# Optimization experiments

Measured on AMD Instinct MI355X. Metric: run time of the kernel, lower is better.

Reference implementation:

```python
import jax, jax.numpy as jnp
import numpy as np

NUM_LAYER = 5
EMB = 300
BN_EPS = 1e-5
NUM_BOND_TYPE = 6
NUM_BOND_DIR = 3
SELF_LOOP_TYPE = 4  # pretrain-gnns self-loop edge attr = [4, 0]


def setup_inputs() -> dict:
    key = jax.random.key(0)
    ks = jax.random.split(key, 12)
    N, E, D = 100000, 250000, EMB
    x = jax.random.normal(ks[0], (N, D), dtype=jnp.float32)
    edge_index = jax.random.randint(ks[1], (2, E), 0, N, dtype=jnp.int64)
    edge_attr = jax.random.randint(ks[2], (E, 2), 0, 3, dtype=jnp.int64)
    L = NUM_LAYER
    W1 = jax.random.normal(ks[3], (L, D, 2 * D), dtype=jnp.float32) * 0.05
    b1 = jnp.zeros((L, 2 * D), dtype=jnp.float32)
    W2 = jax.random.normal(ks[4], (L, 2 * D, D), dtype=jnp.float32) * 0.05
    b2 = jnp.zeros((L, D), dtype=jnp.float32)
    E1 = jax.random.normal(ks[5], (L, NUM_BOND_TYPE, D), dtype=jnp.float32) * 0.05
    E2 = jax.random.normal(ks[6], (L, NUM_BOND_DIR, D), dtype=jnp.float32) * 0.05
    gamma = jnp.ones((L, D), dtype=jnp.float32)
    beta = jnp.zeros((L, D), dtype=jnp.float32)
    return {"x": x, "edge_index": edge_index, "edge_attr": edge_attr,
            "W1": W1, "b1": b1, "W2": W2, "b2": b2,
            "E1": E1, "E2": E2, "gamma": gamma, "beta": beta}


def reference(x, edge_index, edge_attr, W1, b1, W2, b2, E1, E2, gamma, beta):
    N = x.shape[0]
    src, dst = edge_index[0], edge_index[1]
    bt, bd = edge_attr[:, 0], edge_attr[:, 1]
    h = x
    for l in range(NUM_LAYER):
        # GINEConv: message = x_j + edge_embedding, aggr='add', with self loops
        edge_emb = E1[l][bt] + E2[l][bd]                 # [E, D]
        self_emb = E1[l][SELF_LOOP_TYPE] + E2[l][0]      # [D]
        msg = h[src] + edge_emb                          # [E, D] gather
        agg = jax.ops.segment_sum(msg, dst, num_segments=N) + h + self_emb
        # update MLP: Linear(D,2D) -> ReLU -> Linear(2D,D)
        m = jax.nn.relu(agg @ W1[l] + b1[l]) @ W2[l] + b2[l]
        # BatchNorm1d in training mode (batch stats over nodes, biased var)
        mu = m.mean(axis=0)
        var = m.var(axis=0)
        m = (m - mu) * jax.lax.rsqrt(var + BN_EPS) * gamma[l] + beta[l]
        if l < NUM_LAYER - 1:  # ReLU on all but last layer; dropout ratio 0 -> no-op
            m = jax.nn.relu(m)
        h = m
    return h  # JK == 'last'
```

## Files before the change

### kernel.cpp

```cpp
#include <hip/hip_runtime.h>
#include <hip/hip_bf16.h>

#define NN 100000
#define NE 250000
#define DD 300
#define DDB 304
#define NL 5
#define MPAD 100096
#define KA1 320
#define N1 608
#define N1T 640
#define K2 608
#define N2T 384
#define NBLK 391
#define NCMB 19

typedef __attribute__((ext_vector_type(8))) short short8;
typedef __attribute__((ext_vector_type(4))) float f32x4;

#define GLBP(x) ((const __attribute__((address_space(1))) unsigned int*)(x))
#define LDSP(x) ((__attribute__((address_space(3))) unsigned int*)(x))
#define WAITV(N) asm volatile("s_waitcnt vmcnt(" #N ")" ::: "memory")

__device__ __forceinline__ ushort f2bf(float f){
  unsigned u = __float_as_uint(f);
  u += 0x7FFFu + ((u >> 16) & 1u);
  return (ushort)(u >> 16);
}
__device__ __forceinline__ float bf2f(ushort h){
  return __uint_as_float((unsigned)h << 16);
}
__device__ __forceinline__ unsigned pk2(float a, float b){
  return (unsigned)f2bf(a) | ((unsigned)f2bf(b) << 16);
}

__global__ void prep_weights(const float* __restrict__ W1, const float* __restrict__ W2,
                             ushort* __restrict__ W1T, ushort* __restrict__ W2T){
  int idx = blockIdx.x * 256 + threadIdx.x;
  const int total1 = NL * N1T * KA1;
  const int total2 = NL * N2T * K2;
  if (idx < total1){
    int l = idx / (N1T * KA1);
    int rem = idx % (N1T * KA1);
    int n = rem / KA1, k = rem % KA1;
    float v = (n < 2*DD && k < DD) ? W1[(size_t)l*DD*2*DD + (size_t)k*2*DD + n] : 0.0f;
    W1T[idx] = f2bf(v);
  } else {
    int idx2 = idx - total1;
    if (idx2 < total2){
      int l = idx2 / (N2T * K2);
      int rem = idx2 % (N2T * K2);
      int n = rem / K2, k = rem % K2;
      float v = (n < DD && k < 2*DD) ? W2[(size_t)l*2*DD*DD + (size_t)k*DD + n] : 0.0f;
      W2T[idx2] = f2bf(v);
    }
  }
}

__global__ void prep_ctab(const float* __restrict__ E1, const float* __restrict__ E2,
                          float* __restrict__ ctab){
  int idx = blockIdx.x * 256 + threadIdx.x;
  if (idx >= NL * NCMB * DDB) return;
  int l = idx / (NCMB * DDB);
  int rem = idx % (NCMB * DDB);
  int c = rem / DDB, d = rem % DDB;
  float v = 0.0f;
  if (d < DD){
    int bt = (c < 18) ? (c / 3) : 4;
    int bd = (c < 18) ? (c % 3) : 0;
    v = E1[(size_t)l*6*DD + bt*DD + d] + E2[(size_t)l*3*DD + bd*DD + d];
  }
  ctab[idx] = v;
}

__global__ void csr_count(const int* __restrict__ ei, int* __restrict__ deg){
  int e = blockIdx.x * 256 + threadIdx.x;
  if (e < NE) atomicAdd(&deg[ei[NE + e]], 1);
}

__global__ void scan_blk(const int* __restrict__ deg, int* __restrict__ rs, int* __restrict__ bsum){
  __shared__ int tmp[256];
  int i = blockIdx.x * 256 + threadIdx.x;
  int v = (i < NN) ? deg[i] : 0;
  tmp[threadIdx.x] = v;
  __syncthreads();
  #pragma unroll
  for (int off = 1; off < 256; off <<= 1){
    int t = (threadIdx.x >= off) ? tmp[threadIdx.x - off] : 0;
    __syncthreads();
    tmp[threadIdx.x] += t;
    __syncthreads();
  }
  if (i < NN) rs[i] = tmp[threadIdx.x] - v;
  if (threadIdx.x == 255) bsum[blockIdx.x] = tmp[255];
}

__global__ void scan_top(int* __restrict__ bsum){
  __shared__ int tmp[512];
  int v = (threadIdx.x < NBLK) ? bsum[threadIdx.x] : 0;
  tmp[threadIdx.x] = v;
  __syncthreads();
  #pragma unroll
  for (int off = 1; off < 512; off <<= 1){
    int t = (threadIdx.x >= off) ? tmp[threadIdx.x - off] : 0;
    __syncthreads();
    tmp[threadIdx.x] += t;
    __syncthreads();
  }
  if (threadIdx.x < NBLK) bsum[threadIdx.x] = tmp[threadIdx.x] - v;
}

__global__ void scan_add(int* __restrict__ rs, const int* __restrict__ bsum){
  int i = blockIdx.x * 256 + threadIdx.x;
  if (i < NN) rs[i] += bsum[blockIdx.x];
  if (i == 0) rs[NN] = NE;
}

__global__ void csr_fill(const int* __restrict__ ei, const int* __restrict__ ea,
                         const int* __restrict__ rs, int* __restrict__ cursor,
                         int* __restrict__ edges){
  int e = blockIdx.x * 256 + threadIdx.x;
  if (e < NE){
    int dst = ei[NE + e];
    int src = ei[e];
    int c = ea[2*e] * 3 + ea[2*e + 1];
    int p = rs[dst] + atomicAdd(&cursor[dst], 1);
    edges[p] = src | (c << 20);
  }
}

template<int HBF>
__global__ __launch_bounds__(256) void gather_agg(
    const void* __restrict__ hp, const float2* __restrict__ ss,
    const float* __restrict__ ctab_l,
    const int* __restrict__ rs, const int* __restrict__ edges,
    ushort* __restrict__ agg)
{
  int lane = threadIdx.x & 63;
  int wq = __builtin_amdgcn_readfirstlane(threadIdx.x >> 6);
  int wid = blockIdx.x * 4 + wq;
  int nw = gridDim.x * 4;
  int dA = lane * 4;
  int dB = 256 + lane * 4;
  bool laneB  = (lane < 16);
  bool validB = (dB < DD);

  float scA[4], shA[4], scB[4], shB[4];
  if (HBF){
    #pragma unroll
    for (int j = 0; j < 4; ++j){
      float2 s = ss[dA + j]; scA[j] = s.x; shA[j] = s.y;
    }
    if (validB){
      #pragma unroll
      for (int j = 0; j < 4; ++j){
        float2 s = ss[dB + j]; scB[j] = s.x; shB[j] = s.y;
      }
    }
  }

  const float*  hf = (const float*)hp;
  const ushort* hb = (const ushort*)hp;
  const float* ctS = ctab_l + 18*DDB;

  for (int row = wid; row < MPAD; row += nw){
    float a0=0,a1=0,a2=0,a3=0, b0=0,b1=0,b2=0,b3=0;
    if (row < NN){
      if (HBF){
        uint2 hw = *(const uint2*)(hb + (size_t)row*DDB + dA);
        a0 = fmaxf(bf2f((ushort)hw.x)*scA[0]+shA[0],0.f)      + ctS[dA+0];
        a1 = fmaxf(bf2f((ushort)(hw.x>>16))*scA[1]+shA[1],0.f)+ ctS[dA+1];
        a2 = fmaxf(bf2f((ushort)hw.y)*scA[2]+shA[2],0.f)      + ctS[dA+2];
        a3 = fmaxf(bf2f((ushort)(hw.y>>16))*scA[3]+shA[3],0.f)+ ctS[dA+3];
        if (validB){
          uint2 hv = *(const uint2*)(hb + (size_t)row*DDB + dB);
          b0 = fmaxf(bf2f((ushort)hv.x)*scB[0]+shB[0],0.f)      + ctS[dB+0];
          b1 = fmaxf(bf2f((ushort)(hv.x>>16))*scB[1]+shB[1],0.f)+ ctS[dB+1];
          b2 = fmaxf(bf2f((ushort)hv.y)*scB[2]+shB[2],0.f)      + ctS[dB+2];
          b3 = fmaxf(bf2f((ushort)(hv.y>>16))*scB[3]+shB[3],0.f)+ ctS[dB+3];
        }
      } else {
        float4 hv = *(const float4*)(hf + (size_t)row*DD + dA);
        a0 = hv.x + ctS[dA+0]; a1 = hv.y + ctS[dA+1];
        a2 = hv.z + ctS[dA+2]; a3 = hv.w + ctS[dA+3];
        if (validB){
          float4 hv2 = *(const float4*)(hf + (size_t)row*DD + dB);
          b0 = hv2.x + ctS[dB+0]; b1 = hv2.y + ctS[dB+1];
          b2 = hv2.z + ctS[dB+2]; b3 = hv2.w + ctS[dB+3];
        }
      }
      int p = rs[row], pe = rs[row + 1];
      for (; p < pe; ++p){
        int ew = edges[p];
        int src = ew & 0xFFFFF;
        const float* ct = ctab_l + (ew >> 20)*DDB;
        if (HBF){
          uint2 hw = *(const uint2*)(hb + (size_t)src*DDB + dA);
          a0 += fmaxf(bf2f((ushort)hw.x)*scA[0]+shA[0],0.f)      + ct[dA+0];
          a1 += fmaxf(bf2f((ushort)(hw.x>>16))*scA[1]+shA[1],0.f)+ ct[dA+1];
          a2 += fmaxf(bf2f((ushort)hw.y)*scA[2]+shA[2],0.f)      + ct[dA+2];
          a3 += fmaxf(bf2f((ushort)(hw.y>>16))*scA[3]+shA[3],0.f)+ ct[dA+3];
          if (validB){
            uint2 hv = *(const uint2*)(hb + (size_t)src*DDB + dB);
            b0 += fmaxf(bf2f((ushort)hv.x)*scB[0]+shB[0],0.f)      + ct[dB+0];
            b1 += fmaxf(bf2f((ushort)(hv.x>>16))*scB[1]+shB[1],0.f)+ ct[dB+1];
            b2 += fmaxf(bf2f((ushort)hv.y)*scB[2]+shB[2],0.f)      + ct[dB+2];
            b3 += fmaxf(bf2f((ushort)(hv.y>>16))*scB[3]+shB[3],0.f)+ ct[dB+3];
          }
        } else {
          float4 hv = *(const float4*)(hf + (size_t)src*DD + dA);
          a0 += hv.x + ct[dA+0]; a1 += hv.y + ct[dA+1];
          a2 += hv.z + ct[dA+2]; a3 += hv.w + ct[dA+3];
          if (validB){
            float4 hv2 = *(const float4*)(hf + (size_t)src*DD + dB);
            b0 += hv2.x + ct[dB+0]; b1 += hv2.y + ct[dB+1];
            b2 += hv2.z + ct[dB+2]; b3 += hv2.w + ct[dB+3];
          }
        }
      }
    }
    ushort* ag = agg + (size_t)row*KA1;
    uint2 oA; oA.x = pk2(a0, a1); oA.y = pk2(a2, a3);
    *(uint2*)(ag + dA) = oA;
    if (laneB){
      uint2 oB;
      if (validB){ oB.x = pk2(b0, b1); oB.y = pk2(b2, b3); }
      else       { oB.x = 0; oB.y = 0; }
      *(uint2*)(ag + dB) = oB;
    }
  }
}

template<int OUT_BF16, int RELU, int STATS>
__global__ __launch_bounds__(256) void gemm_lds(
    const ushort* __restrict__ A, int lda,
    const ushort* __restrict__ B, int ldb,
    void* __restrict__ Cp, int ldc,
    int kTiles, const float* __restrict__ bias, int biasN,
    int Mvalid, int Nvalid, int nColTiles, float* __restrict__ statf)
{
  __shared__ ushort As[5][4096];
  __shared__ ushort Bs[5][4096];
  int tid = threadIdx.x;
  int lane = tid & 63, w = tid >> 6;
  int wm = (w >> 1) * 64, wn = (w & 1) * 64;

  int nwg = gridDim.x;
  int q = nwg >> 3, r = nwg & 7;
  int xcd = blockIdx.x & 7, idx = blockIdx.x >> 3;
  int bid = (xcd < r ? xcd * (q + 1) : r * (q + 1) + (xcd - r) * q) + idx;
  int m0 = (bid / nColTiles) * 128;
  int n0 = (bid % nColTiles) * 128;

  int r0 = tid >> 2;
  int kc = ((tid & 3) ^ ((tid >> 3) & 3)) * 8;
  const ushort* Ap = A + (size_t)(m0 + r0)*lda + kc;
  const ushort* Bp = B + (size_t)(n0 + r0)*ldb + kc;

  f32x4 acc[4][4] = {};

#define STAGE(buf, kt) do { \
    int _ko = (kt) * 32; \
    __builtin_amdgcn_global_load_lds(GLBP(Ap + _ko),                  LDSP(&As[buf][w*512]),        16, 0, 0); \
    __builtin_amdgcn_global_load_lds(GLBP(Ap + _ko + (size_t)64*lda), LDSP(&As[buf][w*512 + 2048]), 16, 0, 0); \
    __builtin_amdgcn_global_load_lds(GLBP(Bp + _ko),                  LDSP(&Bs[buf][w*512]),        16, 0, 0); \
    __builtin_amdgcn_global_load_lds(GLBP(Bp + _ko + (size_t)64*ldb), LDSP(&Bs[buf][w*512 + 2048]), 16, 0, 0); \
  } while (0)

  STAGE(0, 0); STAGE(1, 1); STAGE(2, 2); STAGE(3, 3);
  WAITV(12);
  __builtin_amdgcn_s_barrier();

  int fr = lane & 15;
  int ko8 = (((lane >> 4) ^ ((fr >> 1) & 3))) * 8;
  int cur = 0;
  for (int kt = 0; kt < kTiles; ++kt){
    int sb = cur + 4; if (sb >= 5) sb -= 5;
    if (kt + 4 < kTiles) STAGE(sb, kt + 4);
    short8 af[4], bfv[4];
    #pragma unroll
    for (int i = 0; i < 4; ++i)
      af[i] = *(const short8*)&As[cur][(wm + i*16 + fr)*32 + ko8];
    #pragma unroll
    for (int j = 0; j < 4; ++j)
      bfv[j] = *(const short8*)&Bs[cur][(wn + j*16 + fr)*32 + ko8];
    #pragma unroll
    for (int i = 0; i < 4; ++i)
      #pragma unroll
      for (int j = 0; j < 4; ++j)
        acc[i][j] = __builtin_amdgcn_mfma_f32_16x16x32_bf16(af[i], bfv[j], acc[i][j], 0, 0, 0);
    if (kt + 1 < kTiles){
      int rem = kTiles - kt;
      if      (rem >= 5) WAITV(12);
      else if (rem == 4) WAITV(8);
      else if (rem == 3) WAITV(4);
      else               WAITV(0);
      __builtin_amdgcn_s_barrier();
    }
    cur = cur + 1; if (cur >= 5) cur = 0;
  }
#undef STAGE

  int cc = lane & 15, cr = (lane >> 4) * 4;
  float ps[4], pq[4];
  if (STATS){
    #pragma unroll
    for (int j = 0; j < 4; ++j){ ps[j] = 0.0f; pq[j] = 0.0f; }
  }
  #pragma unroll
  for (int i = 0; i < 4; ++i){
    #pragma unroll
    for (int j = 0; j < 4; ++j){
      int col = n0 + wn + j*16 + cc;
      if (col >= Nvalid) continue;
      float bv = (col < biasN) ? bias[col] : 0.0f;
      #pragma unroll
      for (int r2 = 0; r2 < 4; ++r2){
        int row = m0 + wm + i*16 + cr + r2;
        if (row < Mvalid){
          float v = acc[i][j][r2] + bv;
          if (RELU) v = fmaxf(v, 0.0f);
          if (OUT_BF16) ((ushort*)Cp)[(size_t)row*ldc + col] = f2bf(v);
          else          ((float*) Cp)[(size_t)row*ldc + col] = v;
          if (STATS){ ps[j] += v; pq[j] += v * v; }
        }
      }
    }
  }
  if (STATS){
    #pragma unroll
    for (int j = 0; j < 4; ++j){
      float s = ps[j], qv = pq[j];
      s += __shfl_xor(s, 16); qv += __shfl_xor(qv, 16);
      s += __shfl_xor(s, 32); qv += __shfl_xor(qv, 32);
      int col = n0 + wn + j*16 + cc;
      if ((lane >> 4) == 0 && col < Nvalid){
        unsafeAtomicAdd(&statf[col], s);
        unsafeAtomicAdd(&statf[N2T + col], qv);
      }
    }
  }
}

__global__ void make_norm(const float* __restrict__ statf, const float* __restrict__ gamma,
                          const float* __restrict__ beta, float2* __restrict__ ss){
  int d = threadIdx.x;
  if (d >= DD) return;
  double mu = (double)statf[d] / (double)NN;
  double var = (double)statf[N2T + d] / (double)NN - mu * mu;
  float inv = rsqrtf((float)var + 1e-5f);
  float sc = inv * gamma[d];
  ss[d] = make_float2(sc, beta[d] - (float)mu * sc);
}

__global__ void apply_norm(const float* __restrict__ m2, const float2* __restrict__ ss,
                           float* __restrict__ out){
  int row = blockIdx.x;
  int d = threadIdx.x;
  if (d >= DD) return;
  float2 s = ss[d];
  out[(size_t)row*DD + d] = m2[(size_t)row*DD + d] * s.x + s.y;
}

extern "C" void kernel_launch(void* const* d_in, const int* in_sizes, int n_in,
                              void* d_out, int out_size, void* d_ws, size_t ws_size,
                              hipStream_t stream) {
  const float* x     = (const float*)d_in[0];
  const int*   ei    = (const int*)  d_in[1];
  const int*   ea    = (const int*)  d_in[2];
  const float* W1    = (const float*)d_in[3];
  const float* b1    = (const float*)d_in[4];
  const float* W2    = (const float*)d_in[5];
  const float* b2    = (const float*)d_in[6];
  const float* E1    = (const float*)d_in[7];
  const float* E2    = (const float*)d_in[8];
  const float* gamma = (const float*)d_in[9];
  const float* beta  = (const float*)d_in[10];

  char* p = (char*)d_ws;
  float*  m2buf = (float*) p; p += (size_t)NN * DD * 4;
  ushort* m2bf  = (ushort*)p; p += (size_t)NN * DDB * 2;
  ushort* agg   = (ushort*)p; p += (size_t)MPAD * KA1 * 2;
  ushort* m1    = (ushort*)p; p += (size_t)MPAD * N1 * 2;
  ushort* W1T   = (ushort*)p; p += (size_t)NL * N1T * KA1 * 2;
  ushort* W2T   = (ushort*)p; p += (size_t)NL * N2T * K2 * 2;
  float*  ctab  = (float*) p; p += (size_t)NL * NCMB * DDB * 4;
  int*    deg   = (int*)   p; p += (size_t)NN * 4;
  int*    rs    = (int*)   p; p += (size_t)(NN + 16) * 4;
  int*    bsum  = (int*)   p; p += (size_t)512 * 4;
  int*    cursor= (int*)   p; p += (size_t)NN * 4;
  int*    edges = (int*)   p; p += (size_t)NE * 4;
  float*  statf = (float*) p; p += (size_t)2 * N2T * 4;
  float2* ss    = (float2*)p;

  {
    int total = NL*N1T*KA1 + NL*N2T*K2;
    prep_weights<<<(total + 255)/256, 256, 0, stream>>>(W1, W2, W1T, W2T);
    int tc = NL * NCMB * DDB;
    prep_ctab<<<(tc + 255)/256, 256, 0, stream>>>(E1, E2, ctab);
  }
  hipMemsetAsync(deg, 0, (size_t)NN*4, stream);
  hipMemsetAsync(cursor, 0, (size_t)NN*4, stream);
  csr_count<<<(NE + 255)/256, 256, 0, stream>>>(ei, deg);
  scan_blk<<<NBLK, 256, 0, stream>>>(deg, rs, bsum);
  scan_top<<<1, 512, 0, stream>>>(bsum);
  scan_add<<<NBLK, 256, 0, stream>>>(rs, bsum);
  csr_fill<<<(NE + 255)/256, 256, 0, stream>>>(ei, ea, rs, cursor, edges);

  for (int l = 0; l < NL; ++l){
    const float* ctab_l = ctab + (size_t)l * NCMB * DDB;

    if (l == 0)
      gather_agg<0><<<1024, 256, 0, stream>>>(x, nullptr, ctab_l, rs, edges, agg);
    else
      gather_agg<1><<<1024, 256, 0, stream>>>(m2bf, ss, ctab_l, rs, edges, agg);

    gemm_lds<1,1,0><<<(MPAD/128) * (N1T/128), 256, 0, stream>>>(
        agg, KA1, W1T + (size_t)l*N1T*KA1, KA1, m1, N1, KA1/32,
        b1 + (size_t)l*2*DD, 2*DD, MPAD, N1, N1T/128, nullptr);

    hipMemsetAsync(statf, 0, (size_t)2*N2T*4, stream);

    if (l < NL - 1)
      gemm_lds<1,0,1><<<(MPAD/128) * (N2T/128), 256, 0, stream>>>(
          m1, N1, W2T + (size_t)l*N2T*K2, K2, m2bf, DDB, K2/32,
          b2 + (size_t)l*DD, DD, NN, DD, N2T/128, statf);
    else
      gemm_lds<0,0,1><<<(MPAD/128) * (N2T/128), 256, 0, stream>>>(
          m1, N1, W2T + (size_t)l*N2T*K2, K2, m2buf, DD, K2/32,
          b2 + (size_t)l*DD, DD, NN, DD, N2T/128, statf);

    make_norm<<<1, 320, 0, stream>>>(statf, gamma + (size_t)l*DD, beta + (size_t)l*DD, ss);
  }
  apply_norm<<<NN, 320, 0, stream>>>(m2buf, ss, (float*)d_out);
}
```

Before: 1.888 ms.

## Add 256-row GEMM tile variant for second MLP layer and double gather grid

Adds a 512-thread GEMM kernel with 256x128 output tiles and a 3-stage LDS pipeline, used for the second MLP linear layer (K=608, N=384). Each B tile is now shared by twice as many rows, and the grid has fewer workgroups. The gather/aggregate kernel launch also doubles from 1024 to 2048 blocks to expose more parallelism. The costs are a shallower pipeline (3 stages instead of 5) and more LDS per block, which may lower occupancy.

```diff
diff --git a/kernel.cpp b/kernel.cpp
--- a/kernel.cpp
+++ b/kernel.cpp
@@ -232,7 +232,7 @@
 }
 
 template<int OUT_BF16, int RELU, int STATS>
-__global__ __launch_bounds__(256) void gemm_lds(
+__global__ __launch_bounds__(256) void gemm_128(
     const ushort* __restrict__ A, int lda,
     const ushort* __restrict__ B, int ldb,
     void* __restrict__ Cp, int ldc,
@@ -298,6 +298,114 @@
       __builtin_amdgcn_s_barrier();
     }
     cur = cur + 1; if (cur >= 5) cur = 0;
+  }
+#undef STAGE
+
+  int cc = lane & 15, cr = (lane >> 4) * 4;
+  float ps[4], pq[4];
+  if (STATS){
+    #pragma unroll
+    for (int j = 0; j < 4; ++j){ ps[j] = 0.0f; pq[j] = 0.0f; }
+  }
+  #pragma unroll
+  for (int i = 0; i < 4; ++i){
+    #pragma unroll
+    for (int j = 0; j < 4; ++j){
+      int col = n0 + wn + j*16 + cc;
+      if (col >= Nvalid) continue;
+      float bv = (col < biasN) ? bias[col] : 0.0f;
+      #pragma unroll
+      for (int r2 = 0; r2 < 4; ++r2){
+        int row = m0 + wm + i*16 + cr + r2;
+        if (row < Mvalid){
+          float v = acc[i][j][r2] + bv;
+          if (RELU) v = fmaxf(v, 0.0f);
+          if (OUT_BF16) ((ushort*)Cp)[(size_t)row*ldc + col] = f2bf(v);
+          else          ((float*) Cp)[(size_t)row*ldc + col] = v;
+          if (STATS){ ps[j] += v; pq[j] += v * v; }
+        }
+      }
+    }
+  }
+  if (STATS){
+    #pragma unroll
+    for (int j = 0; j < 4; ++j){
+      float s = ps[j], qv = pq[j];
+      s += __shfl_xor(s, 16); qv += __shfl_xor(qv, 16);
+      s += __shfl_xor(s, 32); qv += __shfl_xor(qv, 32);
+      int col = n0 + wn + j*16 + cc;
+      if ((lane >> 4) == 0 && col < Nvalid){
+        unsafeAtomicAdd(&statf[col], s);
+        unsafeAtomicAdd(&statf[N2T + col], qv);
+      }
+    }
+  }
+}
+
+template<int OUT_BF16, int RELU, int STATS>
+__global__ __launch_bounds__(512) void gemm_256(
+    const ushort* __restrict__ A, int lda,
+    const ushort* __restrict__ B, int ldb,
+    void* __restrict__ Cp, int ldc,
+    int kTiles, const float* __restrict__ bias, int biasN,
+    int Mvalid, int Nvalid, int nColTiles, float* __restrict__ statf)
+{
+  __shared__ ushort As[3][8192];
+  __shared__ ushort Bs[3][4096];
+  int tid = threadIdx.x;
+  int lane = tid & 63, w = tid >> 6;
+  int wm = (w >> 1) * 64, wn = (w & 1) * 64;
+
+  int nwg = gridDim.x;
+  int q = nwg >> 3, r = nwg & 7;
+  int xcd = blockIdx.x & 7, idx = blockIdx.x >> 3;
+  int bid = (xcd < r ? xcd * (q + 1) : r * (q + 1) + (xcd - r) * q) + idx;
+  int m0 = (bid / nColTiles) * 256;
+  int n0 = (bid % nColTiles) * 128;
+
+  int r0 = tid >> 2;
+  int kc = ((tid & 3) ^ ((tid >> 3) & 3)) * 8;
+  const ushort* Ap = A + (size_t)(m0 + r0)*lda + kc;
+  const ushort* Bp = B + (size_t)(n0 + r0)*ldb + kc;
+
+  f32x4 acc[4][4] = {};
+
+#define STAGE(buf, kt) do { \
+    int _ko = (kt) * 32; \
+    __builtin_amdgcn_global_load_lds(GLBP(Ap + _ko),                   LDSP(&As[buf][w*512]),        16, 0, 0); \
+    __builtin_amdgcn_global_load_lds(GLBP(Ap + _ko + (size_t)128*lda), LDSP(&As[buf][w*512 + 4096]), 16, 0, 0); \
+    __builtin_amdgcn_global_load_lds(GLBP(Bp + _ko),                   LDSP(&Bs[buf][w*512]),        16, 0, 0); \
+  } while (0)
+
+  STAGE(0, 0);
+  STAGE(1, 1);
+  WAITV(3);
+  __builtin_amdgcn_s_barrier();
+
+  int fr = lane & 15;
+  int ko8 = (((lane >> 4) ^ ((fr >> 1) & 3))) * 8;
+  int cur = 0;
+  for (int kt = 0; kt < kTiles; ++kt){
+    int sb = cur + 2; if (sb >= 3) sb -= 3;
+    if (kt + 2 < kTiles) STAGE(sb, kt + 2);
+    short8 af[4], bfv[4];
+    #pragma unroll
+    for (int i = 0; i < 4; ++i)
+      af[i] = *(const short8*)&As[cur][(wm + i*16 + fr)*32 + ko8];
+    #pragma unroll
+    for (int j = 0; j < 4; ++j)
+      bfv[j] = *(const short8*)&Bs[cur][(wn + j*16 + fr)*32 + ko8];
+    #pragma unroll
+    for (int i = 0; i < 4; ++i)
+      #pragma unroll
+      for (int j = 0; j < 4; ++j)
+        acc[i][j] = __builtin_amdgcn_mfma_f32_16x16x32_bf16(af[i], bfv[j], acc[i][j], 0, 0, 0);
+    if (kt + 1 < kTiles){
+      if (kt + 2 < kTiles) WAITV(3);
+      else                 WAITV(0);
+      __builtin_amdgcn_s_barrier();
+    }
+    cur = cur + 1; if (cur >= 3) cur = 0;
   }
 #undef STAGE
 
@@ -411,22 +519,22 @@
     const float* ctab_l = ctab + (size_t)l * NCMB * DDB;
 
     if (l == 0)
-      gather_agg<0><<<1024, 256, 0, stream>>>(x, nullptr, ctab_l, rs, edges, agg);
+      gather_agg<0><<<2048, 256, 0, stream>>>(x, nullptr, ctab_l, rs, edges, agg);
     else
-      gather_agg<1><<<1024, 256, 0, stream>>>(m2bf, ss, ctab_l, rs, edges, agg);
-
-    gemm_lds<1,1,0><<<(MPAD/128) * (N1T/128), 256, 0, stream>>>(
+      gather_agg<1><<<2048, 256, 0, stream>>>(m2bf, ss, ctab_l, rs, edges, agg);
+
+    gemm_128<1,1,0><<<(MPAD/128) * (N1T/128), 256, 0, stream>>>(
         agg, KA1, W1T + (size_t)l*N1T*KA1, KA1, m1, N1, KA1/32,
         b1 + (size_t)l*2*DD, 2*DD, MPAD, N1, N1T/128, nullptr);
 
     hipMemsetAsync(statf, 0, (size_t)2*N2T*4, stream);
 
     if (l < NL - 1)
-      gemm_lds<1,0,1><<<(MPAD/128) * (N2T/128), 256, 0, stream>>>(
+      gemm_256<1,0,1><<<(MPAD/256) * (N2T/128), 512, 0, stream>>>(
           m1, N1, W2T + (size_t)l*N2T*K2, K2, m2bf, DDB, K2/32,
           b2 + (size_t)l*DD, DD, NN, DD, N2T/128, statf);
     else
-      gemm_lds<0,0,1><<<(MPAD/128) * (N2T/128), 256, 0, stream>>>(
+      gemm_256<0,0,1><<<(MPAD/256) * (N2T/128), 512, 0, stream>>>(
           m1, N1, W2T + (size_t)l*N2T*K2, K2, m2buf, DD, K2/32,
           b2 + (size_t)l*DD, DD, NN, DD, N2T/128, statf);
 
```

Measured after the change: 1.753 ms. 7.1% less time.

## Fuse the two MLP GEMMs into one kernel keeping the hidden tile in LDS

Applied to the files above, without the earlier changes.

Replaces the two separate GEMM launches with a single 512-thread kernel. Each block owns 128 rows, computes the 640-wide hidden layer in 128-column chunks, applies bias and ReLU into an LDS tile, and accumulates the second GEMM over all 384 output columns in registers. This removes the global round trip of the 100k x 608 bf16 intermediate and one launch per layer. In exchange it needs large LDS and register use, which lowers occupancy, and only 782 blocks are launched. The gather kernel grid is also doubled.

```diff
diff --git a/kernel.cpp b/kernel.cpp
--- a/kernel.cpp
+++ b/kernel.cpp
@@ -8,10 +8,9 @@
 #define NL 5
 #define MPAD 100096
 #define KA1 320
-#define N1 608
 #define N1T 640
-#define K2 608
 #define N2T 384
+#define K2P 640
 #define NBLK 391
 #define NCMB 19
 
@@ -38,7 +37,7 @@
                              ushort* __restrict__ W1T, ushort* __restrict__ W2T){
   int idx = blockIdx.x * 256 + threadIdx.x;
   const int total1 = NL * N1T * KA1;
-  const int total2 = NL * N2T * K2;
+  const int total2 = NL * N2T * K2P;
   if (idx < total1){
     int l = idx / (N1T * KA1);
     int rem = idx % (N1T * KA1);
@@ -48,9 +47,9 @@
   } else {
     int idx2 = idx - total1;
     if (idx2 < total2){
-      int l = idx2 / (N2T * K2);
-      int rem = idx2 % (N2T * K2);
-      int n = rem / K2, k = rem % K2;
+      int l = idx2 / (N2T * K2P);
+      int rem = idx2 % (N2T * K2P);
+      int n = rem / K2P, k = rem % K2P;
       float v = (n < DD && k < 2*DD) ? W2[(size_t)l*2*DD*DD + (size_t)k*DD + n] : 0.0f;
       W2T[idx2] = f2bf(v);
     }
@@ -164,7 +163,7 @@
   const float* ctS = ctab_l + 18*DDB;
 
   for (int row = wid; row < MPAD; row += nw){
-    float a0=0,a1=0,a2=0,a3=0, b0=0,b1=0,b2=0,b3=0;
+    float a0=0,a1=0,a2=0,a3=0, b0=0,b1v=0,b2v=0,b3=0;
     if (row < NN){
       if (HBF){
         uint2 hw = *(const uint2*)(hb + (size_t)row*DDB + dA);
@@ -174,10 +173,10 @@
         a3 = fmaxf(bf2f((ushort)(hw.y>>16))*scA[3]+shA[3],0.f)+ ctS[dA+3];
         if (validB){
           uint2 hv = *(const uint2*)(hb + (size_t)row*DDB + dB);
-          b0 = fmaxf(bf2f((ushort)hv.x)*scB[0]+shB[0],0.f)      + ctS[dB+0];
-          b1 = fmaxf(bf2f((ushort)(hv.x>>16))*scB[1]+shB[1],0.f)+ ctS[dB+1];
-          b2 = fmaxf(bf2f((ushort)hv.y)*scB[2]+shB[2],0.f)      + ctS[dB+2];
-          b3 = fmaxf(bf2f((ushort)(hv.y>>16))*scB[3]+shB[3],0.f)+ ctS[dB+3];
+          b0  = fmaxf(bf2f((ushort)hv.x)*scB[0]+shB[0],0.f)      + ctS[dB+0];
+          b1v = fmaxf(bf2f((ushort)(hv.x>>16))*scB[1]+shB[1],0.f)+ ctS[dB+1];
+          b2v = fmaxf(bf2f((ushort)hv.y)*scB[2]+shB[2],0.f)      + ctS[dB+2];
+          b3  = fmaxf(bf2f((ushort)(hv.y>>16))*scB[3]+shB[3],0.f)+ ctS[dB+3];
         }
       } else {
         float4 hv = *(const float4*)(hf + (size_t)row*DD + dA);
@@ -185,8 +184,8 @@
         a2 = hv.z + ctS[dA+2]; a3 = hv.w + ctS[dA+3];
         if (validB){
           float4 hv2 = *(const float4*)(hf + (size_t)row*DD + dB);
-          b0 = hv2.x + ctS[dB+0]; b1 = hv2.y + ctS[dB+1];
-          b2 = hv2.z + ctS[dB+2]; b3 = hv2.w + ctS[dB+3];
+          b0 = hv2.x + ctS[dB+0]; b1v = hv2.y + ctS[dB+1];
+          b2v = hv2.z + ctS[dB+2]; b3 = hv2.w + ctS[dB+3];
         }
       }
       int p = rs[row], pe = rs[row + 1];
@@ -202,10 +201,10 @@
           a3 += fmaxf(bf2f((ushort)(hw.y>>16))*scA[3]+shA[3],0.f)+ ct[dA+3];
           if (validB){
             uint2 hv = *(const uint2*)(hb + (size_t)src*DDB + dB);
-            b0 += fmaxf(bf2f((ushort)hv.x)*scB[0]+shB[0],0.f)      + ct[dB+0];
-            b1 += fmaxf(bf2f((ushort)(hv.x>>16))*scB[1]+shB[1],0.f)+ ct[dB+1];
-            b2 += fmaxf(bf2f((ushort)hv.y)*scB[2]+shB[2],0.f)      + ct[dB+2];
-            b3 += fmaxf(bf2f((ushort)(hv.y>>16))*scB[3]+shB[3],0.f)+ ct[dB+3];
+            b0  += fmaxf(bf2f((ushort)hv.x)*scB[0]+shB[0],0.f)      + ct[dB+0];
+            b1v += fmaxf(bf2f((ushort)(hv.x>>16))*scB[1]+shB[1],0.f)+ ct[dB+1];
+            b2v += fmaxf(bf2f((ushort)hv.y)*scB[2]+shB[2],0.f)      + ct[dB+2];
+            b3  += fmaxf(bf2f((ushort)(hv.y>>16))*scB[3]+shB[3],0.f)+ ct[dB+3];
           }
         } else {
           float4 hv = *(const float4*)(hf + (size_t)src*DD + dA);
@@ -213,8 +212,8 @@
           a2 += hv.z + ct[dA+2]; a3 += hv.w + ct[dA+3];
           if (validB){
             float4 hv2 = *(const float4*)(hf + (size_t)src*DD + dB);
-            b0 += hv2.x + ct[dB+0]; b1 += hv2.y + ct[dB+1];
-            b2 += hv2.z + ct[dB+2]; b3 += hv2.w + ct[dB+3];
+            b0 += hv2.x + ct[dB+0]; b1v += hv2.y + ct[dB+1];
+            b2v += hv2.z + ct[dB+2]; b3 += hv2.w + ct[dB+3];
           }
         }
       }
@@ -224,120 +223,177 @@
     *(uint2*)(ag + dA) = oA;
     if (laneB){
       uint2 oB;
-      if (validB){ oB.x = pk2(b0, b1); oB.y = pk2(b2, b3); }
+      if (validB){ oB.x = pk2(b0, b1v); oB.y = pk2(b2v, b3); }
       else       { oB.x = 0; oB.y = 0; }
       *(uint2*)(ag + dB) = oB;
     }
   }
 }
 
-template<int OUT_BF16, int RELU, int STATS>
-__global__ __launch_bounds__(256) void gemm_lds(
-    const ushort* __restrict__ A, int lda,
-    const ushort* __restrict__ B, int ldb,
+template<int OUT_BF16>
+__global__ __launch_bounds__(512) void mlp_fused(
+    const ushort* __restrict__ agg,
+    const ushort* __restrict__ W1T_l,
+    const ushort* __restrict__ W2T_l,
+    const float* __restrict__ b1_l,
+    const float* __restrict__ b2_l,
     void* __restrict__ Cp, int ldc,
-    int kTiles, const float* __restrict__ bias, int biasN,
-    int Mvalid, int Nvalid, int nColTiles, float* __restrict__ statf)
+    float* __restrict__ statf)
 {
-  __shared__ ushort As[5][4096];
-  __shared__ ushort Bs[5][4096];
+  __shared__ ushort Sa[3][4096];
+  __shared__ ushort Sb[3][4096];
+  __shared__ ushort Ws[3][12288];
+  __shared__ ushort Pt[16384];
+
   int tid = threadIdx.x;
   int lane = tid & 63, w = tid >> 6;
-  int wm = (w >> 1) * 64, wn = (w & 1) * 64;
+  int wmA = (w >> 2) * 64;
+  int wnA = (w & 3) * 32;
+  int wnB = (w & 3) * 96;
 
   int nwg = gridDim.x;
   int q = nwg >> 3, r = nwg & 7;
-  int xcd = blockIdx.x & 7, idx = blockIdx.x >> 3;
-  int bid = (xcd < r ? xcd * (q + 1) : r * (q + 1) + (xcd - r) * q) + idx;
-  int m0 = (bid / nColTiles) * 128;
-  int n0 = (bid % nColTiles) * 128;
+  int xcd = blockIdx.x & 7, bix = blockIdx.x >> 3;
+  int bid = (xcd < r ? xcd*(q+1) : r*(q+1) + (xcd-r)*q) + bix;
+  int m0 = bid * 128;
 
   int r0 = tid >> 2;
   int kc = ((tid & 3) ^ ((tid >> 3) & 3)) * 8;
-  const ushort* Ap = A + (size_t)(m0 + r0)*lda + kc;
-  const ushort* Bp = B + (size_t)(n0 + r0)*ldb + kc;
-
-  f32x4 acc[4][4] = {};
-
-#define STAGE(buf, kt) do { \
+  const ushort* Ap = agg + (size_t)(m0 + r0)*KA1 + kc;
+
+  int fr = lane & 15;
+  int kq = lane >> 4;
+  int ko8 = (kq ^ ((fr >> 1) & 3)) * 8;
+  int cc = lane & 15, cr = kq * 4;
+
+  f32x4 acc2[4][6] = {};
+
+#define STAGE_A(buf, kt) do { \
     int _ko = (kt) * 32; \
-    __builtin_amdgcn_global_load_lds(GLBP(Ap + _ko),                  LDSP(&As[buf][w*512]),        16, 0, 0); \
-    __builtin_amdgcn_global_load_lds(GLBP(Ap + _ko + (size_t)64*lda), LDSP(&As[buf][w*512 + 2048]), 16, 0, 0); \
-    __builtin_amdgcn_global_load_lds(GLBP(Bp + _ko),                  LDSP(&Bs[buf][w*512]),        16, 0, 0); \
-    __builtin_amdgcn_global_load_lds(GLBP(Bp + _ko + (size_t)64*ldb), LDSP(&Bs[buf][w*512 + 2048]), 16, 0, 0); \
+    __builtin_amdgcn_global_load_lds(GLBP(Ap + _ko),  LDSP(&Sa[buf][w*512]), 16, 0, 0); \
+    __builtin_amdgcn_global_load_lds(GLBP(W1p + _ko), LDSP(&Sb[buf][w*512]), 16, 0, 0); \
   } while (0)
-
-  STAGE(0, 0); STAGE(1, 1); STAGE(2, 2); STAGE(3, 3);
-  WAITV(12);
-  __builtin_amdgcn_s_barrier();
-
-  int fr = lane & 15;
-  int ko8 = (((lane >> 4) ^ ((fr >> 1) & 3))) * 8;
-  int cur = 0;
-  for (int kt = 0; kt < kTiles; ++kt){
-    int sb = cur + 4; if (sb >= 5) sb -= 5;
-    if (kt + 4 < kTiles) STAGE(sb, kt + 4);
-    short8 af[4], bfv[4];
+#define STAGE_W(buf, s) do { \
+    int _ko = (s) * 32; \
+    __builtin_amdgcn_global_load_lds(GLBP(W2p + _ko),                   LDSP(&Ws[buf][w*512]),        16, 0, 0); \
+    __builtin_amdgcn_global_load_lds(GLBP(W2p + _ko + (size_t)128*K2P), LDSP(&Ws[buf][w*512 + 4096]), 16, 0, 0); \
+    __builtin_amdgcn_global_load_lds(GLBP(W2p + _ko + (size_t)256*K2P), LDSP(&Ws[buf][w*512 + 8192]), 16, 0, 0); \
+  } while (0)
+
+  #pragma unroll 1
+  for (int jb = 0; jb < 5; ++jb){
+    const ushort* W1p = W1T_l + (size_t)(jb*128 + r0)*KA1 + kc;
+    const ushort* W2p = W2T_l + (size_t)r0*K2P + jb*128 + kc;
+
+    f32x4 accA[4][2] = {};
+    STAGE_A(0, 0); STAGE_A(1, 1);
+    WAITV(2);
+    __builtin_amdgcn_s_barrier();
+    int cur = 0;
+    for (int kt = 0; kt < 10; ++kt){
+      int sb = cur + 2; if (sb >= 3) sb -= 3;
+      if (kt + 2 < 10) STAGE_A(sb, kt + 2);
+      short8 af[4], bw[2];
+      #pragma unroll
+      for (int i = 0; i < 4; ++i)
+        af[i] = *(const short8*)&Sa[cur][(wmA + i*16 + fr)*32 + ko8];
+      #pragma unroll
+      for (int j2 = 0; j2 < 2; ++j2)
+        bw[j2] = *(const short8*)&Sb[cur][(wnA + j2*16 + fr)*32 + ko8];
+      #pragma unroll
+      for (int i = 0; i < 4; ++i)
+        #pragma unroll
+        for (int j2 = 0; j2 < 2; ++j2)
+          accA[i][j2] = __builtin_amdgcn_mfma_f32_16x16x32_bf16(af[i], bw[j2], accA[i][j2], 0, 0, 0);
+      if (kt + 1 < 10){
+        if (kt + 2 < 10) WAITV(2);
+        else             WAITV(0);
+        __builtin_amdgcn_s_barrier();
+      }
+      cur = cur + 1; if (cur >= 3) cur = 0;
+    }
     #pragma unroll
-    for (int i = 0; i < 4; ++i)
-      af[i] = *(const short8*)&As[cur][(wm + i*16 + fr)*32 + ko8];
+    for (int i = 0; i < 4; ++i){
+      #pragma unroll
+      for (int j2 = 0; j2 < 2; ++j2){
+        int pcol = wnA + j2*16 + cc;
+        int gcol = jb*128 + pcol;
+        float bv = (gcol < 2*DD) ? b1_l[gcol] : 0.0f;
+        #pragma unroll
+        for (int r2 = 0; r2 < 4; ++r2){
+          int prow = wmA + i*16 + cr + r2;
+          float v = fmaxf(accA[i][j2][r2] + bv, 0.0f);
+          int gp = (pcol >> 3) ^ ((prow >> 1) & 7);
+          Pt[prow*128 + gp*8 + (pcol & 7)] = f2bf(v);
+        }
+      }
+    }
+    STAGE_W(0, 0); STAGE_W(1, 1);
+    asm volatile("s_waitcnt lgkmcnt(0)" ::: "memory");
+    __builtin_amdgcn_sched_barrier(0);
+    __builtin_amdgcn_s_barrier();
+    WAITV(3);
+    __builtin_amdgcn_s_barrier();
+
     #pragma unroll
-    for (int j = 0; j < 4; ++j)
-      bfv[j] = *(const short8*)&Bs[cur][(wn + j*16 + fr)*32 + ko8];
-    #pragma unroll
-    for (int i = 0; i < 4; ++i)
-      #pragma unroll
-      for (int j = 0; j < 4; ++j)
-        acc[i][j] = __builtin_amdgcn_mfma_f32_16x16x32_bf16(af[i], bfv[j], acc[i][j], 0, 0, 0);
-    if (kt + 1 < kTiles){
-      int rem = kTiles - kt;
-      if      (rem >= 5) WAITV(12);
-      else if (rem == 4) WAITV(8);
-      else if (rem == 3) WAITV(4);
-      else               WAITV(0);
+    for (int s = 0; s < 4; ++s){
+      if (s + 2 < 4) STAGE_W((s + 2) % 3, s + 2);
+      if      (s == 1) WAITV(6);
+      else if (s == 2) WAITV(3);
+      else if (s == 3) WAITV(0);
+      if (s) __builtin_amdgcn_s_barrier();
+      short8 pf[4], wf[6];
+      #pragma unroll
+      for (int i = 0; i < 4; ++i){
+        int prow = wmA + i*16 + fr;
+        int gp = (s*4 + kq) ^ ((prow >> 1) & 7);
+        pf[i] = *(const short8*)&Pt[prow*128 + gp*8];
+      }
+      #pragma unroll
+      for (int j2 = 0; j2 < 6; ++j2)
+        wf[j2] = *(const short8*)&Ws[s % 3][(wnB + j2*16 + fr)*32 + ko8];
+      #pragma unroll
+      for (int i = 0; i < 4; ++i)
+        #pragma unroll
+        for (int j2 = 0; j2 < 6; ++j2)
+          acc2[i][j2] = __builtin_amdgcn_mfma_f32_16x16x32_bf16(pf[i], wf[j2], acc2[i][j2], 0, 0, 0);
       __builtin_amdgcn_s_barrier();
     }
-    cur = cur + 1; if (cur >= 5) cur = 0;
-  }
-#undef STAGE
-
-  int cc = lane & 15, cr = (lane >> 4) * 4;
-  float ps[4], pq[4];
-  if (STATS){
-    #pragma unroll
-    for (int j = 0; j < 4; ++j){ ps[j] = 0.0f; pq[j] = 0.0f; }
-  }
+  }
+#undef STAGE_A
+#undef STAGE_W
+
+  float ps[6], pq[6];
+  #pragma unroll
+  for (int j2 = 0; j2 < 6; ++j2){ ps[j2] = 0.0f; pq[j2] = 0.0f; }
   #pragma unroll
   for (int i = 0; i < 4; ++i){
     #pragma unroll
-    for (int j = 0; j < 4; ++j){
-      int col = n0 + wn + j*16 + cc;
-      if (col >= Nvalid) continue;
-      float bv = (col < biasN) ? bias[col] : 0.0f;
+    for (int j2 = 0; j2 < 6; ++j2){
+      int col = wnB + j2*16 + cc;
+      if (col >= DD) continue;
+      float bv = b2_l[col];
       #pragma unroll
       for (int r2 = 0; r2 < 4; ++r2){
-        int row = m0 + wm + i*16 + cr + r2;
-        if (row < Mvalid){
-          float v = acc[i][j][r2] + bv;
-          if (RELU) v = fmaxf(v, 0.0f);
+        int row = m0 + wmA + i*16 + cr + r2;
+        if (row < NN){
+          float v = acc2[i][j2][r2] + bv;
           if (OUT_BF16) ((ushort*)Cp)[(size_t)row*ldc + col] = f2bf(v);
           else          ((float*) Cp)[(size_t)row*ldc + col] = v;
-          if (STATS){ ps[j] += v; pq[j] += v * v; }
+          ps[j2] += v; pq[j2] += v * v;
         }
       }
     }
   }
-  if (STATS){
-    #pragma unroll
-    for (int j = 0; j < 4; ++j){
-      float s = ps[j], qv = pq[j];
-      s += __shfl_xor(s, 16); qv += __shfl_xor(qv, 16);
-      s += __shfl_xor(s, 32); qv += __shfl_xor(qv, 32);
-      int col = n0 + wn + j*16 + cc;
-      if ((lane >> 4) == 0 && col < Nvalid){
-        unsafeAtomicAdd(&statf[col], s);
-        unsafeAtomicAdd(&statf[N2T + col], qv);
-      }
+  #pragma unroll
+  for (int j2 = 0; j2 < 6; ++j2){
+    float s = ps[j2], qv = pq[j2];
+    s += __shfl_xor(s, 16); qv += __shfl_xor(qv, 16);
+    s += __shfl_xor(s, 32); qv += __shfl_xor(qv, 32);
+    int col = wnB + j2*16 + cc;
+    if (kq == 0 && col < DD){
+      unsafeAtomicAdd(&statf[col], s);
+      unsafeAtomicAdd(&statf[N2T + col], qv);
     }
   }
 }
@@ -381,9 +437,8 @@
   float*  m2buf = (float*) p; p += (size_t)NN * DD * 4;
   ushort* m2bf  = (ushort*)p; p += (size_t)NN * DDB * 2;
   ushort* agg   = (ushort*)p; p += (size_t)MPAD * KA1 * 2;
-  ushort* m1    = (ushort*)p; p += (size_t)MPAD * N1 * 2;
   ushort* W1T   = (ushort*)p; p += (size_t)NL * N1T * KA1 * 2;
-  ushort* W2T   = (ushort*)p; p += (size_t)NL * N2T * K2 * 2;
+  ushort* W2T   = (ushort*)p; p += (size_t)NL * N2T * K2P * 2;
   float*  ctab  = (float*) p; p += (size_t)NL * NCMB * DDB * 4;
   int*    deg   = (int*)   p; p += (size_t)NN * 4;
   int*    rs    = (int*)   p; p += (size_t)(NN + 16) * 4;
@@ -394,7 +449,7 @@
   float2* ss    = (float2*)p;
 
   {
-    int total = NL*N1T*KA1 + NL*N2T*K2;
+    int total = NL*N1T*KA1 + NL*N2T*K2P;
     prep_weights<<<(total + 255)/256, 256, 0, stream>>>(W1, W2, W1T, W2T);
     int tc = NL * NCMB * DDB;
     prep_ctab<<<(tc + 255)/256, 256, 0, stream>>>(E1, E2, ctab);
@@ -411,24 +466,20 @@
     const float* ctab_l = ctab + (size_t)l * NCMB * DDB;
 
     if (l == 0)
-      gather_agg<0><<<1024, 256, 0, stream>>>(x, nullptr, ctab_l, rs, edges, agg);
+      gather_agg<0><<<2048, 256, 0, stream>>>(x, nullptr, ctab_l, rs, edges, agg);
     else
-      gather_agg<1><<<1024, 256, 0, stream>>>(m2bf, ss, ctab_l, rs, edges, agg);
-
-    gemm_lds<1,1,0><<<(MPAD/128) * (N1T/128), 256, 0, stream>>>(
-        agg, KA1, W1T + (size_t)l*N1T*KA1, KA1, m1, N1, KA1/32,
-        b1 + (size_t)l*2*DD, 2*DD, MPAD, N1, N1T/128, nullptr);
+      gather_agg<1><<<2048, 256, 0, stream>>>(m2bf, ss, ctab_l, rs, edges, agg);
 
     hipMemsetAsync(statf, 0, (size_t)2*N2T*4, stream);
 
     if (l < NL - 1)
-      gemm_lds<1,0,1><<<(MPAD/128) * (N2T/128), 256, 0, stream>>>(
-          m1, N1, W2T + (size_t)l*N2T*K2, K2, m2bf, DDB, K2/32,
-          b2 + (size_t)l*DD, DD, NN, DD, N2T/128, statf);
+      mlp_fused<1><<<MPAD/128, 512, 0, stream>>>(
+          agg, W1T + (size_t)l*N1T*KA1, W2T + (size_t)l*N2T*K2P,
+          b1 + (size_t)l*2*DD, b2 + (size_t)l*DD, m2bf, DDB, statf);
     else
-      gemm_lds<0,0,1><<<(MPAD/128) * (N2T/128), 256, 0, stream>>>(
-          m1, N1, W2T + (size_t)l*N2T*K2, K2, m2buf, DD, K2/32,
-          b2 + (size_t)l*DD, DD, NN, DD, N2T/128, statf);
+      mlp_fused<0><<<MPAD/128, 512, 0, stream>>>(
+          agg, W1T + (size_t)l*N1T*KA1, W2T + (size_t)l*N2T*K2P,
+          b1 + (size_t)l*2*DD, b2 + (size_t)l*DD, m2buf, DD, statf);
 
     make_norm<<<1, 320, 0, stream>>>(statf, gamma + (size_t)l*DD, beta + (size_t)l*DD, ss);
   }
```

After: 1.706 ms. -9.6%, faster.
